# Optimization experiments

Measured on AMD Instinct MI355X. Metric: run time of the kernel, lower is better.

The kernel has to match this reference:

```python
import jax, jax.numpy as jnp
import numpy as np


def conv(x, w, b, stride=1):
    # x: [N,C,H,W], w: [O,I,3,3] (torch OIHW), pad=1
    y = jax.lax.conv_general_dilated(x, w, (stride, stride), ((1, 1), (1, 1)),
                                     dimension_numbers=('NCHW', 'OIHW', 'NCHW'))
    return y + b[None, :, None, None]


def backward_warp(frame, flow):
    # Replicates F.grid_sample(mode='bilinear', padding_mode='border', align_corners=False)
    # with the base grid linspace(-1+1/W, 1-1/W, W) and flow normalized by (W-1)/2, (H-1)/2.
    N, C, H, W = frame.shape
    gx = jnp.linspace(-1.0 + 1.0 / W, 1.0 - 1.0 / W, W, dtype=frame.dtype)[None, None, :] \
         + flow[:, 0] / ((W - 1.0) / 2.0)   # [N,H,W] normalized x
    gy = jnp.linspace(-1.0 + 1.0 / H, 1.0 - 1.0 / H, H, dtype=frame.dtype)[None, :, None] \
         + flow[:, 1] / ((H - 1.0) / 2.0)   # [N,H,W] normalized y
    # align_corners=False un-normalization, then border clamp
    x = jnp.clip(((gx + 1.0) * W - 1.0) / 2.0, 0.0, W - 1.0)
    y = jnp.clip(((gy + 1.0) * H - 1.0) / 2.0, 0.0, H - 1.0)
    x0 = jnp.floor(x); y0 = jnp.floor(y)
    wx = (x - x0)[:, None]; wy = (y - y0)[:, None]   # [N,1,H,W]
    ix0 = x0.astype(jnp.int32); iy0 = y0.astype(jnp.int32)
    ix1 = jnp.minimum(ix0 + 1, W - 1); iy1 = jnp.minimum(iy0 + 1, H - 1)
    gather = jax.vmap(lambda fr, iy, ix: fr[:, iy, ix])  # per-sample [C,H,W] gather
    v00 = gather(frame, iy0, ix0); v01 = gather(frame, iy0, ix1)
    v10 = gather(frame, iy1, ix0); v11 = gather(frame, iy1, ix1)
    return (v00 * (1 - wx) * (1 - wy) + v01 * wx * (1 - wy)
            + v10 * (1 - wx) * wy + v11 * wx * wy)


def up2x(x):
    # F.interpolate(scale_factor=2, mode='bilinear', align_corners=False)
    N, C, H, W = x.shape
    return jax.image.resize(x, (N, C, 2 * H, 2 * W), method='bilinear')


def forward_fn(img0, img1, ft0, ft1, ft0_s2, ft1_s2, ft0_s4, ft1_s4,
               c0_0, c0_1, c0_2, c1_0, c1_1, c1_2,
               wd0a, bd0a, wd0b, bd0b, wd1a, bd1a, wd1b, bd1b,
               wd2a, bd2a, wd2b, bd2b, wu0, bu0, wu1, bu1, wu2, bu2, wfin, bfin):
    relu = jax.nn.relu
    # down0: [N,70,H,W] -> [N,32,H/2,W/2]
    s0_in = jnp.concatenate([img0, img1, backward_warp(c0_0, ft0), backward_warp(c1_0, ft1)], axis=1)
    s0 = relu(conv(relu(conv(s0_in, wd0a, bd0a, 2)), wd0b, bd0b))
    # down1: [N,128,H/2,W/2] -> [N,64,H/4,W/4]
    s1_in = jnp.concatenate([s0, backward_warp(c0_1, ft0_s2), backward_warp(c1_1, ft1_s2)], axis=1)
    s1 = relu(conv(relu(conv(s1_in, wd1a, bd1a, 2)), wd1b, bd1b))
    # down2: [N,192,H/4,W/4] -> [N,96,H/8,W/8]
    s2_in = jnp.concatenate([s1, backward_warp(c0_2, ft0_s4), backward_warp(c1_2, ft1_s4)], axis=1)
    s2 = relu(conv(relu(conv(s2_in, wd2a, bd2a, 2)), wd2b, bd2b))
    # decoder with skip concats; each up block is Sequential(ReLU, Conv, ReLU)
    x = relu(conv(relu(up2x(s2)), wu0, bu0))
    x = relu(conv(relu(up2x(jnp.concatenate([x, s1], axis=1))), wu1, bu1))
    x = relu(conv(relu(up2x(jnp.concatenate([x, s0], axis=1))), wu2, bu2))
    return conv(x, wfin, bfin)  # [N,4,H,W]


def setup_inputs() -> dict:
    key = jax.random.key(0)
    ks = iter(jax.random.split(key, 64))
    N, H, W = 4, 384, 384
    f32 = jnp.float32
    inp = {
        'img0': jax.random.uniform(next(ks), (N, 3, H, W), f32),
        'img1': jax.random.uniform(next(ks), (N, 3, H, W), f32),
        'ft0': jax.random.normal(next(ks), (N, 2, H, W), f32),
        'ft1': jax.random.normal(next(ks), (N, 2, H, W), f32),
        'ft0_s2': jax.random.normal(next(ks), (N, 2, H // 2, W // 2), f32),
        'ft1_s2': jax.random.normal(next(ks), (N, 2, H // 2, W // 2), f32),
        'ft0_s4': jax.random.normal(next(ks), (N, 2, H // 4, W // 4), f32),
        'ft1_s4': jax.random.normal(next(ks), (N, 2, H // 4, W // 4), f32),
        'c0_0': jax.random.normal(next(ks), (N, 32, H, W), f32),
        'c0_1': jax.random.normal(next(ks), (N, 48, H // 2, W // 2), f32),
        'c0_2': jax.random.normal(next(ks), (N, 64, H // 4, W // 4), f32),
        'c1_0': jax.random.normal(next(ks), (N, 32, H, W), f32),
        'c1_1': jax.random.normal(next(ks), (N, 48, H // 2, W // 2), f32),
        'c1_2': jax.random.normal(next(ks), (N, 64, H // 4, W // 4), f32),
    }
    # conv weights, torch OIHW layout; input_dim = 3*2 + 32*2 = 70
    shapes = {
        'wd0a': (32, 70, 3, 3), 'wd0b': (32, 32, 3, 3),
        'wd1a': (64, 128, 3, 3), 'wd1b': (64, 64, 3, 3),
        'wd2a': (96, 192, 3, 3), 'wd2b': (96, 96, 3, 3),
        'wu0': (64, 96, 3, 3), 'wu1': (32, 128, 3, 3), 'wu2': (70, 64, 3, 3),
        'wfin': (4, 70, 3, 3),
    }
    for name, shp in shapes.items():
        fan_in = shp[1] * 9
        inp[name] = jax.random.normal(next(ks), shp, f32) * (1.0 / np.sqrt(fan_in))
        inp['b' + name[1:]] = jax.random.normal(next(ks), (shp[0],), f32) * 0.01
    return inp


def reference(img0, img1, ft0, ft1, ft0_s2, ft1_s2, ft0_s4, ft1_s4,
              c0_0, c0_1, c0_2, c1_0, c1_1, c1_2,
              wd0a, bd0a, wd0b, bd0b, wd1a, bd1a, wd1b, bd1b,
              wd2a, bd2a, wd2b, bd2b, wu0, bu0, wu1, bu1, wu2, bu2, wfin, bfin):
    return forward_fn(img0, img1, ft0, ft1, ft0_s2, ft1_s2, ft0_s4, ft1_s4,
                      c0_0, c0_1, c0_2, c1_0, c1_1, c1_2,
                      wd0a, bd0a, wd0b, bd0b, wd1a, bd1a, wd1b, bd1b,
                      wd2a, bd2a, wd2b, bd2b, wu0, bu0, wu1, bu1, wu2, bu2, wfin, bfin)
```

## Files before the change

kernel.cpp:

```cpp
#include <hip/hip_runtime.h>

#define DIV_UP(a,b) (((a)+(b)-1)/(b))

typedef unsigned short u16;
typedef __attribute__((ext_vector_type(8))) short s8v;
typedef __attribute__((ext_vector_type(4))) float f4v;
typedef __attribute__((ext_vector_type(2))) unsigned int u2v;

__device__ __forceinline__ float b2f(u16 x) {
    return __uint_as_float(((unsigned)x) << 16);
}
__device__ __forceinline__ u16 f2b(float f) {
    unsigned u = __float_as_uint(f);
    return (u16)((u + 0x7FFFu + ((u >> 16) & 1u)) >> 16);
}

#define GLD16(gp, lp) __builtin_amdgcn_global_load_lds( \
    (const __attribute__((address_space(1))) unsigned int*)(gp), \
    (__attribute__((address_space(3))) unsigned int*)(lp), 16, 0, 0)

struct HZ { u16* p; int H, W, C; };
struct HZ6 { HZ d[6]; };
__global__ __launch_bounds__(256) void halo_zero(HZ6 Z)
{
    HZ d = Z.d[blockIdx.y];
    int pw = d.W + 2, ph = d.H + 2;
    int tot = 4 * ph * pw;
    int idx = blockIdx.x * 256 + threadIdx.x;
    if (idx >= tot) return;
    int r = idx % (ph * pw);
    int y = r / pw, x = r - y * pw;
    if (y > 0 && y <= d.H && x > 0 && x <= d.W) return;
    u16* p = d.p + (size_t)idx * d.C;
    s8v z = {0,0,0,0,0,0,0,0};
    for (int c = 0; c < d.C; c += 8) *(s8v*)(p + c) = z;
}

struct WT { const float* src; u16* dst; int Cout, Cin, COUTP, CINP, shift; };
struct WT10 { WT d[10]; };
__global__ __launch_bounds__(256) void wtrans(WT10 Z)
{
    WT d = Z.d[blockIdx.y];
    int tot = 9 * d.COUTP * d.CINP;
    int idx = blockIdx.x * 256 + threadIdx.x;
    if (idx >= tot) return;
    int s = idx / (d.COUTP * d.CINP);
    int r = idx - s * (d.COUTP * d.CINP);
    int co = r / d.CINP, ci = r - co * d.CINP;
    int sci = ci;
    bool ok = (co < d.Cout);
    if (d.shift) {
        if (ci < 6)                 sci = ci;
        else if (ci >= 8 && ci < 72) sci = ci - 2;
        else                        ok = false;
    }
    ok = ok && (sci < d.Cin);
    float v = ok ? d.src[((size_t)co * d.Cin + sci) * 9 + s] : 0.f;
    d.dst[idx] = f2b(v);
}

__global__ __launch_bounds__(256) void img_cat(
    const float* __restrict__ i0, const float* __restrict__ i1, u16* __restrict__ dst)
{
    int idx = blockIdx.x * 256 + threadIdx.x;
    if (idx >= 4 * 147456) return;
    int n = idx / 147456, r = idx - n * 147456;
    int y = r / 384, x = r - y * 384;
    u16* p = dst + ((size_t)n * 386 * 386 + (size_t)(y + 1) * 386 + (x + 1)) * 72;
#pragma unroll
    for (int c = 0; c < 3; ++c) {
        p[c]     = f2b(i0[((size_t)(n * 3 + c)) * 147456 + r]);
        p[3 + c] = f2b(i1[((size_t)(n * 3 + c)) * 147456 + r]);
    }
    p[6] = 0; p[7] = 0;
}

__global__ __launch_bounds__(256) void t_nhwc(
    const float* __restrict__ src, u16* __restrict__ dst, int C, int HW, int total)
{
    int idx = blockIdx.x * 256 + threadIdx.x;
    if (idx >= total) return;
    int n = idx / HW, p = idx - n * HW;
    const float* s = src + (size_t)n * C * HW + p;
    u16* d = dst + (size_t)idx * C;
    for (int c8 = 0; c8 < C; c8 += 8) {
        s8v v;
#pragma unroll
        for (int i = 0; i < 8; ++i)
            v[i] = (short)f2b(s[(size_t)(c8 + i) * HW]);
        *(s8v*)(d + c8) = v;
    }
}

__global__ __launch_bounds__(256) void warp_nhwc(
    const u16* __restrict__ fr, const float* __restrict__ flow,
    u16* __restrict__ dst, int chb, int C, int H, int W, int CALLOC, int total)
{
    int HW = H * W;
    int idx = blockIdx.x * 256 + threadIdx.x;
    if (idx >= total) return;
    int n = idx / HW, r = idx - n * HW;
    int i = r / W, j = r - i * W;

    float fx = flow[((size_t)n * 2 + 0) * HW + r];
    float fy = flow[((size_t)n * 2 + 1) * HW + r];
    float x = (float)j + fx * ((float)W / (float)(W - 1));
    float y = (float)i + fy * ((float)H / (float)(H - 1));
    x = fminf(fmaxf(x, 0.f), (float)(W - 1));
    y = fminf(fmaxf(y, 0.f), (float)(H - 1));
    float x0f = floorf(x), y0f = floorf(y);
    int ix0 = (int)x0f, iy0 = (int)y0f;
    int ix1 = ix0 + 1; if (ix1 > W - 1) ix1 = W - 1;
    int iy1 = iy0 + 1; if (iy1 > H - 1) iy1 = H - 1;
    float wx = x - x0f, wy = y - y0f;
    float w00 = (1.f - wx) * (1.f - wy), w01 = wx * (1.f - wy);
    float w10 = (1.f - wx) * wy,         w11 = wx * wy;

    const u16* fb  = fr + (size_t)n * HW * C;
    const u16* p00 = fb + (size_t)(iy0 * W + ix0) * C;
    const u16* p01 = fb + (size_t)(iy0 * W + ix1) * C;
    const u16* p10 = fb + (size_t)(iy1 * W + ix0) * C;
    const u16* p11 = fb + (size_t)(iy1 * W + ix1) * C;
    u16* db = dst + ((size_t)n * (H + 2) * (W + 2) + (size_t)(i + 1) * (W + 2) + (j + 1)) * CALLOC + chb;

    for (int c8 = 0; c8 < C; c8 += 8) {
        s8v a = *(const s8v*)(p00 + c8);
        s8v b = *(const s8v*)(p01 + c8);
        s8v c = *(const s8v*)(p10 + c8);
        s8v d = *(const s8v*)(p11 + c8);
        s8v o;
#pragma unroll
        for (int t = 0; t < 8; ++t)
            o[t] = (short)f2b(w00 * b2f((u16)a[t]) + w01 * b2f((u16)b[t])
                            + w10 * b2f((u16)c[t]) + w11 * b2f((u16)d[t]));
        *(s8v*)(db + c8) = o;
    }
}

template<int CINP, int CHUNK, int CIN_ALLOC, int COUTP, int COUT, int STORE_LIM,
         int HO, int WO, int HT, int STRIDE, int RELU, int SRC_MODE, int OUT_MODE, int OCALLOC>
__global__ __launch_bounds__(256) void conv_k(
    const u16* __restrict__ srcA, const u16* __restrict__ srcB,
    long nsA, int rsA, int cA, long nsB, int rsB, int cB, int splitC,
    const u16* __restrict__ wt, const float* __restrict__ bias,
    void* __restrict__ outv)
{
    constexpr int WROWS = (HT == 16) ? 4 : 1;
    constexpr int ROWS  = (STRIDE == 1) ? HT + 2 : 2 * HT + 1;
    constexpr int COLS  = (STRIDE == 1) ? 18 : 33;
    constexpr int SUBS  = CHUNK / 8;
    constexpr int LSUB  = (SUBS == 8) ? 3 : 2;
    constexpr int XM    = SUBS - 1;
    constexpr int CH2   = CHUNK * 2;
    constexpr int NCHK  = CINP / CHUNK;
    constexpr int KK    = CHUNK / 32;
    constexpr int MT    = COUTP / 16;
    constexpr int NPX   = ROWS * COLS;
    constexpr int IN_B  = NPX * CH2;
    constexpr int W_B   = COUTP * CH2;
    constexpr int WI    = WO * STRIDE;
    constexpr int Hs    = HO / 2, Ws = WO / 2;
    constexpr long NSO  = (OUT_MODE == 0) ? (long)(HO + 2) * (WO + 2) * OCALLOC
                                          : (long)HO * WO * OCALLOC;

    __shared__ s8v ldsv[(IN_B + 2 * W_B) / 16];
    char* lds  = (char*)ldsv;
    char* ldw0 = lds + IN_B;
    char* ldw1 = ldw0 + W_B;

    const int tid  = threadIdx.x;
    const int wv   = tid >> 6;
    const int lane = tid & 63;
    const int lr   = lane & 15;
    const int koct = lane >> 4;
    const int bx   = blockIdx.x, n = blockIdx.z;
    const int tx   = (bx % (WO / 16)) * 16;
    const int ty   = (bx / (WO / 16)) * HT;

    f4v acc[MT][WROWS];
#pragma unroll
    for (int m = 0; m < MT; ++m)
#pragma unroll
        for (int r = 0; r < WROWS; ++r) acc[m][r] = (f4v){0.f, 0.f, 0.f, 0.f};

    float bv[MT][4];
#pragma unroll
    for (int m = 0; m < MT; ++m)
#pragma unroll
        for (int j = 0; j < 4; ++j) {
            int co = m * 16 + koct * 4 + j;
            bv[m][j] = (co < COUT) ? bias[co] : 0.f;
        }

    for (int cig = 0; cig < NCHK; ++cig) {
        if (cig) __syncthreads();

        if constexpr (SRC_MODE == 0) {
            const u16* ns = srcA + (size_t)n * nsA;
            if (CIN_ALLOC >= CINP || (cig + 1) * CHUNK <= CIN_ALLOC) {
                for (int t = tid; t < NPX * SUBS; t += 256) {
                    int q = t >> LSUB, sub = t & XM;
                    int iy = q / COLS, ix = q - iy * COLS;
                    int xr = (STRIDE == 1) ? (q & XM) : ((q >> 1) & XM);
                    int ci0 = cig * CHUNK + (sub ^ xr) * 8;
                    const u16* g = ns + ((size_t)(ty * STRIDE + iy) * (WI + 2)
                                         + (tx * STRIDE + ix)) * CIN_ALLOC + ci0;
                    GLD16(g, lds + t * 16);
                }
            } else {
                for (int t = tid; t < NPX * SUBS; t += 256) {
                    int q = t >> LSUB, sub = t & XM;
                    int iy = q / COLS, ix = q - iy * COLS;
                    int xr = (STRIDE == 1) ? (q & XM) : ((q >> 1) & XM);
                    int ci0 = cig * CHUNK + (sub ^ xr) * 8;
                    s8v v = {0,0,0,0,0,0,0,0};
                    if (ci0 < CIN_ALLOC)
                        v = *(const s8v*)(ns + ((size_t)(ty * STRIDE + iy) * (WI + 2)
                                                + (tx * STRIDE + ix)) * CIN_ALLOC + ci0);
                    *(s8v*)(lds + t * 16) = v;
                }
            }
        } else {
            for (int t = tid; t < NPX * SUBS; t += 256) {
                int q = t >> LSUB, sub = t & XM;
                int iy = q / COLS, ix = q - iy * COLS;
                int ssub = sub ^ (q & XM);
                int ci0 = cig * CHUNK + ssub * 8;
                int gy = ty + iy - 1, gx = tx + ix - 1;
                s8v val = {0,0,0,0,0,0,0,0};
                if ((unsigned)gy < (unsigned)HO && (unsigned)gx < (unsigned)WO) {
                    const u16* sp; int rs, cal, cof; long nss;
                    if (ci0 < splitC) { sp = srcA; nss = nsA; rs = rsA; cal = cA; cof = ci0; }
                    else              { sp = srcB; nss = nsB; rs = rsB; cal = cB; cof = ci0 - splitC; }
                    sp += (size_t)n * nss;
                    float fy = ((float)gy + 0.5f) * 0.5f - 0.5f;
                    float fx = ((float)gx + 0.5f) * 0.5f - 0.5f;
                    float y0f = floorf(fy), x0f = floorf(fx);
                    float wy = fy - y0f, wx = fx - x0f;
                    int y0 = (int)y0f, x0 = (int)x0f;
                    int y1 = y0 + 1, x1 = x0 + 1;
                    y0 = max(y0, 0); x0 = max(x0, 0);
                    y1 = min(y1, Hs - 1); x1 = min(x1, Ws - 1);
                    const s8v a = *(const s8v*)(sp + (size_t)y0 * rs + (size_t)x0 * cal + cof);
                    const s8v b = *(const s8v*)(sp + (size_t)y0 * rs + (size_t)x1 * cal + cof);
                    const s8v c = *(const s8v*)(sp + (size_t)y1 * rs + (size_t)x0 * cal + cof);
                    const s8v d = *(const s8v*)(sp + (size_t)y1 * rs + (size_t)x1 * cal + cof);
                    float w00 = (1.f - wx) * (1.f - wy), w01 = wx * (1.f - wy);
                    float w10 = (1.f - wx) * wy,         w11 = wx * wy;
#pragma unroll
                    for (int i = 0; i < 8; ++i) {
                        float v = w00 * b2f((u16)a[i]) + w01 * b2f((u16)b[i])
                                + w10 * b2f((u16)c[i]) + w11 * b2f((u16)d[i]);
                        val[i] = (short)f2b(v);
                    }
                }
                *(s8v*)(lds + t * 16) = val;
            }
        }

        auto stageW = [&](int s, char* dstb) {
            for (int t = tid; t < COUTP * SUBS; t += 256) {
                int co = t >> LSUB, sub = t & XM;
                int ssub = sub ^ (co & XM);
                const u16* g = wt + ((size_t)(s * COUTP + co) * CINP + cig * CHUNK + ssub * 8);
                GLD16(g, dstb + t * 16);
            }
        };
        stageW(0, ldw0);

#pragma unroll
        for (int s = 0; s < 9; ++s) {
            __syncthreads();
            if (s < 8) stageW(s + 1, (s & 1) ? ldw0 : ldw1);
            char* wc = (s & 1) ? ldw1 : ldw0;
            const int dy = s / 3, dx = s - dy * 3;
#pragma unroll
            for (int kk = 0; kk < KK; ++kk) {
                const int koff = kk * 64 + koct * 16;
                s8v bfr[WROWS];
#pragma unroll
                for (int r = 0; r < WROWS; ++r) {
                    int orow = wv * WROWS + r;
                    int q, xr;
                    if (STRIDE == 1) { q = (orow + dy) * COLS + lr + dx; xr = q & XM; }
                    else             { q = (2 * orow + dy) * COLS + 2 * lr + dx; xr = (q >> 1) & XM; }
                    bfr[r] = *(const s8v*)(lds + q * CH2 + (koff ^ (xr << 4)));
                }
#pragma unroll
                for (int m = 0; m < MT; ++m) {
                    s8v afr = *(const s8v*)(wc + (m * 16 + lr) * CH2 + (koff ^ ((lr & XM) << 4)));
#pragma unroll
                    for (int r = 0; r < WROWS; ++r)
                        acc[m][r] = __builtin_amdgcn_mfma_f32_16x16x32_bf16(afr, bfr[r], acc[m][r], 0, 0, 0);
                }
            }
        }
    }

#pragma unroll
    for (int m = 0; m < MT; ++m) {
#pragma unroll
        for (int r = 0; r < WROWS; ++r) {
            int row = ty + wv * WROWS + r, col = tx + lr;
            float x0 = acc[m][r][0] + bv[m][0];
            float x1 = acc[m][r][1] + bv[m][1];
            float x2 = acc[m][r][2] + bv[m][2];
            float x3 = acc[m][r][3] + bv[m][3];
            if (RELU) {
                x0 = fmaxf(x0, 0.f); x1 = fmaxf(x1, 0.f);
                x2 = fmaxf(x2, 0.f); x3 = fmaxf(x3, 0.f);
            }
            int co0 = m * 16 + koct * 4;
            if constexpr (OUT_MODE == 2) {
                float* op = (float*)outv;
                float xs[4] = {x0, x1, x2, x3};
#pragma unroll
                for (int j = 0; j < 4; ++j)
                    if (co0 + j < STORE_LIM)
                        op[((size_t)(n * 4 + co0 + j) * HO + row) * WO + col] = xs[j];
            } else {
                size_t pix = (OUT_MODE == 0)
                    ? ((size_t)(row + 1) * (WO + 2) + (col + 1))
                    : ((size_t)row * WO + col);
                u16* ob = (u16*)outv + (size_t)n * NSO + pix * OCALLOC + co0;
                if (co0 + 3 < STORE_LIM) {
                    unsigned lo = (unsigned)f2b(x0) | ((unsigned)f2b(x1) << 16);
                    unsigned hi = (unsigned)f2b(x2) | ((unsigned)f2b(x3) << 16);
                    *(u2v*)ob = (u2v){lo, hi};
                } else {
                    float xs[4] = {x0, x1, x2, x3};
#pragma unroll
                    for (int j = 0; j < 4; ++j)
                        if (co0 + j < STORE_LIM) ob[j] = f2b(xs[j]);
                }
            }
        }
    }
}

extern "C" void kernel_launch(void* const* d_in, const int* in_sizes, int n_in,
                              void* d_out, int out_size, void* d_ws, size_t ws_size,
                              hipStream_t stream)
{
    const float* img0  = (const float*)d_in[0];
    const float* img1  = (const float*)d_in[1];
    const float* ft0   = (const float*)d_in[2];
    const float* ft1   = (const float*)d_in[3];
    const float* ft0s2 = (const float*)d_in[4];
    const float* ft1s2 = (const float*)d_in[5];
    const float* ft0s4 = (const float*)d_in[6];
    const float* ft1s4 = (const float*)d_in[7];
    const float* c0_0  = (const float*)d_in[8];
    const float* c0_1  = (const float*)d_in[9];
    const float* c0_2  = (const float*)d_in[10];
    const float* c1_0  = (const float*)d_in[11];
    const float* c1_1  = (const float*)d_in[12];
    const float* c1_2  = (const float*)d_in[13];
    const float* wd0a = (const float*)d_in[14]; const float* bd0a = (const float*)d_in[15];
    const float* wd0b = (const float*)d_in[16]; const float* bd0b = (const float*)d_in[17];
    const float* wd1a = (const float*)d_in[18]; const float* bd1a = (const float*)d_in[19];
    const float* wd1b = (const float*)d_in[20]; const float* bd1b = (const float*)d_in[21];
    const float* wd2a = (const float*)d_in[22]; const float* bd2a = (const float*)d_in[23];
    const float* wd2b = (const float*)d_in[24]; const float* bd2b = (const float*)d_in[25];
    const float* wu0  = (const float*)d_in[26]; const float* bu0  = (const float*)d_in[27];
    const float* wu1  = (const float*)d_in[28]; const float* bu1  = (const float*)d_in[29];
    const float* wu2  = (const float*)d_in[30]; const float* bu2  = (const float*)d_in[31];
    const float* wfin = (const float*)d_in[32]; const float* bfin = (const float*)d_in[33];

    u16* ws = (u16*)d_ws;
    u16* s0in = ws + 0;
    u16* x2   = ws + 0;
    u16* s1in = ws + 42913152;
    u16* s2in = ws + 62182784;
    u16* scr  = ws + 69558656;
    u16* t0   = ws + 69558656;
    u16* t1   = ws + 74376064;
    u16* t2   = ws + 76834688;
    u16* s2b  = ws + 77794688;
    u16* x0   = ws + 78679424;
    u16* x1   = ws + 81038720;
    u16* wtb  = ws + 85757312;
    u16* Wd0a = wtb;
    u16* Wd0b = Wd0a + 27648;
    u16* Wd1a = Wd0b + 9216;
    u16* Wd1b = Wd1a + 73728;
    u16* Wd2a = Wd1b + 36864;
    u16* Wd2b = Wd2a + 165888;
    u16* Wu0  = Wd2b + 82944;
    u16* Wu1  = Wu0 + 55296;
    u16* Wu2  = Wu1 + 36864;
    u16* Wfin = Wu2 + 46080;

    const int HW384 = 147456, HW192 = 36864, HW96 = 9216;

    for (int f = 0; f < 2; ++f) {
        const float* fr = f ? c1_0 : c0_0;
        const float* fl = f ? ft1 : ft0;
        int chb = f ? 40 : 8;
        for (int n = 0; n < 4; ++n) {
            t_nhwc<<<DIV_UP(HW384, 256), 256, 0, stream>>>(
                fr + (size_t)n * 32 * HW384, scr, 32, HW384, HW384);
            warp_nhwc<<<DIV_UP(HW384, 256), 256, 0, stream>>>(
                scr, fl + (size_t)n * 2 * HW384,
                s0in + (size_t)n * 386 * 386 * 72, chb, 32, 384, 384, 72, HW384);
        }
    }
    for (int f = 0; f < 2; ++f) {
        t_nhwc<<<DIV_UP(4 * HW192, 256), 256, 0, stream>>>(
            f ? c1_1 : c0_1, scr, 48, HW192, 4 * HW192);
        warp_nhwc<<<DIV_UP(4 * HW192, 256), 256, 0, stream>>>(
            scr, f ? ft1s2 : ft0s2, s1in, f ? 80 : 32, 48, 192, 192, 128, 4 * HW192);
    }
    for (int f = 0; f < 2; ++f) {
        t_nhwc<<<DIV_UP(4 * HW96, 256), 256, 0, stream>>>(
            f ? c1_2 : c0_2, scr, 64, HW96, 4 * HW96);
        warp_nhwc<<<DIV_UP(4 * HW96, 256), 256, 0, stream>>>(
            scr, f ? ft1s4 : ft0s4, s2in, f ? 128 : 64, 64, 96, 96, 192, 4 * HW96);
    }

    HZ6 hz = {{ {s0in, 384, 384, 72}, {s1in, 192, 192, 128}, {s2in, 96, 96, 192},
                {t0, 192, 192, 32},   {t1, 96, 96, 64},      {t2, 48, 48, 96} }};
    halo_zero<<<dim3(DIV_UP(4 * 386 * 386, 256), 6), 256, 0, stream>>>(hz);

    WT10 wt = {{ {wd0a, Wd0a, 32, 70, 32, 96, 1},  {wd0b, Wd0b, 32, 32, 32, 32, 0},
                 {wd1a, Wd1a, 64, 128, 64, 128, 0},{wd1b, Wd1b, 64, 64, 64, 64, 0},
                 {wd2a, Wd2a, 96, 192, 96, 192, 0},{wd2b, Wd2b, 96, 96, 96, 96, 0},
                 {wu0,  Wu0,  64, 96, 64, 96, 0},  {wu1,  Wu1,  32, 128, 32, 128, 0},
                 {wu2,  Wu2,  70, 64, 80, 64, 0},  {wfin, Wfin, 4, 70, 16, 96, 0} }};
    wtrans<<<dim3(DIV_UP(9 * 96 * 192, 256), 10), 256, 0, stream>>>(wt);

    img_cat<<<DIV_UP(4 * 147456, 256), 256, 0, stream>>>(img0, img1, s0in);

    conv_k<96,32,72, 32,32,32, 192,192,4,2,1, 0,0,32>
        <<<dim3(12*48,1,4),256,0,stream>>>(s0in,nullptr, 386L*386*72,0,0, 0,0,0,0, Wd0a,bd0a,t0);
    conv_k<32,32,32, 32,32,32, 192,192,16,1,1, 0,0,128>
        <<<dim3(12*12,1,4),256,0,stream>>>(t0,nullptr, 194L*194*32,0,0, 0,0,0,0, Wd0b,bd0b,s1in);

    conv_k<128,32,128, 64,64,64, 96,96,4,2,1, 0,0,64>
        <<<dim3(6*24,1,4),256,0,stream>>>(s1in,nullptr, 194L*194*128,0,0, 0,0,0,0, Wd1a,bd1a,t1);
    conv_k<64,64,64, 64,64,64, 96,96,4,1,1, 0,0,192>
        <<<dim3(6*24,1,4),256,0,stream>>>(t1,nullptr, 98L*98*64,0,0, 0,0,0,0, Wd1b,bd1b,s2in);

    conv_k<192,32,192, 96,96,96, 48,48,4,2,1, 0,0,96>
        <<<dim3(3*12,1,4),256,0,stream>>>(s2in,nullptr, 98L*98*192,0,0, 0,0,0,0, Wd2a,bd2a,t2);
    conv_k<96,32,96, 96,96,96, 48,48,4,1,1, 0,1,96>
        <<<dim3(3*12,1,4),256,0,stream>>>(t2,nullptr, 50L*50*96,0,0, 0,0,0,0, Wd2b,bd2b,s2b);

    conv_k<96,32,96, 64,64,64, 96,96,4,1,1, 1,1,64>
        <<<dim3(6*24,1,4),256,0,stream>>>(s2b,s2b, 48L*48*96,48*96,96, 48L*48*96,48*96,96, 96,
                                          Wu0,bu0,x0);
    conv_k<128,64,128, 32,32,32, 192,192,16,1,1, 1,1,32>
        <<<dim3(12*12,1,4),256,0,stream>>>(x0, s2in + (size_t)(98+1)*192,
                                           96L*96*64,96*64,64, 98L*98*192,98*192,192, 64,
                                           Wu1,bu1,x1);
    conv_k<64,64,64, 80,70,70, 384,384,16,1,1, 1,0,72>
        <<<dim3(24*24,1,4),256,0,stream>>>(x1, s1in + (size_t)(194+1)*128,
                                           192L*192*32,192*32,32, 194L*194*128,194*128,128, 32,
                                           Wu2,bu2,x2);

    conv_k<96,32,72, 16,4,4, 384,384,16,1,0, 0,2,0>
        <<<dim3(24*24,1,4),256,0,stream>>>(x2,nullptr, 386L*386*72,0,0, 0,0,0,0, Wfin,bfin,d_out);
}
```

Measured before the change: 797.7 us.

## Materialize upsampled inputs and read conv weights directly from global memory

Moves the bilinear 2x upsample and skip-concatenation out of the conv loader into a separate kernel that writes a zero-padded upsampled buffer, so the up-path convs use the plain padded loader. It also removes the double-buffered LDS staging of weights: MFMA A-fragments are now loaded straight from global memory, with one barrier per channel chunk instead of one per tap. The intent is to cut loader arithmetic and synchronisation. In exchange it adds large intermediate write/read traffic and uncached global weight reads inside the inner loop.

```diff
diff --git a/kernel.cpp b/kernel.cpp
--- a/kernel.cpp
+++ b/kernel.cpp
@@ -137,11 +137,56 @@
     }
 }
 
+__global__ __launch_bounds__(256) void up2x_mat(
+    const u16* __restrict__ A, long nsA, int rsA, int cA,
+    const u16* __restrict__ B, long nsB, int rsB, int cB, int splitC,
+    u16* __restrict__ out, int C, int Hs, int Ws)
+{
+    int Ho = 2 * Hs, Wo = 2 * Ws;
+    int pw = Wo + 2, ph = Ho + 2;
+    int tot = 4 * ph * pw;
+    int idx = blockIdx.x * 256 + threadIdx.x;
+    if (idx >= tot) return;
+    int n = idx / (ph * pw), r = idx - n * (ph * pw);
+    int py = r / pw, px = r - py * pw;
+    u16* d = out + (size_t)idx * C;
+    int gy = py - 1, gx = px - 1;
+    if ((unsigned)gy >= (unsigned)Ho || (unsigned)gx >= (unsigned)Wo) {
+        s8v z = {0,0,0,0,0,0,0,0};
+        for (int c8 = 0; c8 < C; c8 += 8) *(s8v*)(d + c8) = z;
+        return;
+    }
+    float fy = ((float)gy + 0.5f) * 0.5f - 0.5f;
+    float fx = ((float)gx + 0.5f) * 0.5f - 0.5f;
+    float y0f = floorf(fy), x0f = floorf(fx);
+    float wy = fy - y0f, wx = fx - x0f;
+    int y0 = max((int)y0f, 0), x0 = max((int)x0f, 0);
+    int y1 = min((int)y0f + 1, Hs - 1), x1 = min((int)x0f + 1, Ws - 1);
+    float w00 = (1.f - wx) * (1.f - wy), w01 = wx * (1.f - wy);
+    float w10 = (1.f - wx) * wy,         w11 = wx * wy;
+
+    for (int c8 = 0; c8 < C; c8 += 8) {
+        const u16* sp; int rs, cal, cof; long nss;
+        if (c8 < splitC) { sp = A; nss = nsA; rs = rsA; cal = cA; cof = c8; }
+        else              { sp = B; nss = nsB; rs = rsB; cal = cB; cof = c8 - splitC; }
+        sp += (size_t)n * nss;
+        const s8v a = *(const s8v*)(sp + (size_t)y0 * rs + (size_t)x0 * cal + cof);
+        const s8v b = *(const s8v*)(sp + (size_t)y0 * rs + (size_t)x1 * cal + cof);
+        const s8v c = *(const s8v*)(sp + (size_t)y1 * rs + (size_t)x0 * cal + cof);
+        const s8v e = *(const s8v*)(sp + (size_t)y1 * rs + (size_t)x1 * cal + cof);
+        s8v o;
+#pragma unroll
+        for (int i = 0; i < 8; ++i)
+            o[i] = (short)f2b(w00 * b2f((u16)a[i]) + w01 * b2f((u16)b[i])
+                            + w10 * b2f((u16)c[i]) + w11 * b2f((u16)e[i]));
+        *(s8v*)(d + c8) = o;
+    }
+}
+
 template<int CINP, int CHUNK, int CIN_ALLOC, int COUTP, int COUT, int STORE_LIM,
          int HO, int WO, int HT, int STRIDE, int RELU, int SRC_MODE, int OUT_MODE, int OCALLOC>
 __global__ __launch_bounds__(256) void conv_k(
-    const u16* __restrict__ srcA, const u16* __restrict__ srcB,
-    long nsA, int rsA, int cA, long nsB, int rsB, int cB, int splitC,
+    const u16* __restrict__ src, long ns,
     const u16* __restrict__ wt, const float* __restrict__ bias,
     void* __restrict__ outv)
 {
@@ -157,16 +202,12 @@
     constexpr int MT    = COUTP / 16;
     constexpr int NPX   = ROWS * COLS;
     constexpr int IN_B  = NPX * CH2;
-    constexpr int W_B   = COUTP * CH2;
     constexpr int WI    = WO * STRIDE;
-    constexpr int Hs    = HO / 2, Ws = WO / 2;
     constexpr long NSO  = (OUT_MODE == 0) ? (long)(HO + 2) * (WO + 2) * OCALLOC
                                           : (long)HO * WO * OCALLOC;
 
-    __shared__ s8v ldsv[(IN_B + 2 * W_B) / 16];
-    char* lds  = (char*)ldsv;
-    char* ldw0 = lds + IN_B;
-    char* ldw1 = ldw0 + W_B;
+    __shared__ s8v ldsv[IN_B / 16];
+    char* lds = (char*)ldsv;
 
     const int tid  = threadIdx.x;
     const int wv   = tid >> 6;
@@ -195,16 +236,16 @@
     for (int cig = 0; cig < NCHK; ++cig) {
         if (cig) __syncthreads();
 
+        const u16* nsrc = src + (size_t)n * ns;
         if constexpr (SRC_MODE == 0) {
-            const u16* ns = srcA + (size_t)n * nsA;
             if (CIN_ALLOC >= CINP || (cig + 1) * CHUNK <= CIN_ALLOC) {
                 for (int t = tid; t < NPX * SUBS; t += 256) {
                     int q = t >> LSUB, sub = t & XM;
                     int iy = q / COLS, ix = q - iy * COLS;
                     int xr = (STRIDE == 1) ? (q & XM) : ((q >> 1) & XM);
                     int ci0 = cig * CHUNK + (sub ^ xr) * 8;
-                    const u16* g = ns + ((size_t)(ty * STRIDE + iy) * (WI + 2)
-                                         + (tx * STRIDE + ix)) * CIN_ALLOC + ci0;
+                    const u16* g = nsrc + ((size_t)(ty * STRIDE + iy) * (WI + 2)
+                                           + (tx * STRIDE + ix)) * CIN_ALLOC + ci0;
                     GLD16(g, lds + t * 16);
                 }
             } else {
@@ -215,8 +256,8 @@
                     int ci0 = cig * CHUNK + (sub ^ xr) * 8;
                     s8v v = {0,0,0,0,0,0,0,0};
                     if (ci0 < CIN_ALLOC)
-                        v = *(const s8v*)(ns + ((size_t)(ty * STRIDE + iy) * (WI + 2)
-                                                + (tx * STRIDE + ix)) * CIN_ALLOC + ci0);
+                        v = *(const s8v*)(nsrc + ((size_t)(ty * STRIDE + iy) * (WI + 2)
+                                                  + (tx * STRIDE + ix)) * CIN_ALLOC + ci0);
                     *(s8v*)(lds + t * 16) = v;
                 }
             }
@@ -224,56 +265,20 @@
             for (int t = tid; t < NPX * SUBS; t += 256) {
                 int q = t >> LSUB, sub = t & XM;
                 int iy = q / COLS, ix = q - iy * COLS;
-                int ssub = sub ^ (q & XM);
-                int ci0 = cig * CHUNK + ssub * 8;
+                int xr = q & XM;
+                int ci0 = cig * CHUNK + (sub ^ xr) * 8;
                 int gy = ty + iy - 1, gx = tx + ix - 1;
-                s8v val = {0,0,0,0,0,0,0,0};
-                if ((unsigned)gy < (unsigned)HO && (unsigned)gx < (unsigned)WO) {
-                    const u16* sp; int rs, cal, cof; long nss;
-                    if (ci0 < splitC) { sp = srcA; nss = nsA; rs = rsA; cal = cA; cof = ci0; }
-                    else              { sp = srcB; nss = nsB; rs = rsB; cal = cB; cof = ci0 - splitC; }
-                    sp += (size_t)n * nss;
-                    float fy = ((float)gy + 0.5f) * 0.5f - 0.5f;
-                    float fx = ((float)gx + 0.5f) * 0.5f - 0.5f;
-                    float y0f = floorf(fy), x0f = floorf(fx);
-                    float wy = fy - y0f, wx = fx - x0f;
-                    int y0 = (int)y0f, x0 = (int)x0f;
-                    int y1 = y0 + 1, x1 = x0 + 1;
-                    y0 = max(y0, 0); x0 = max(x0, 0);
-                    y1 = min(y1, Hs - 1); x1 = min(x1, Ws - 1);
-                    const s8v a = *(const s8v*)(sp + (size_t)y0 * rs + (size_t)x0 * cal + cof);
-                    const s8v b = *(const s8v*)(sp + (size_t)y0 * rs + (size_t)x1 * cal + cof);
-                    const s8v c = *(const s8v*)(sp + (size_t)y1 * rs + (size_t)x0 * cal + cof);
-                    const s8v d = *(const s8v*)(sp + (size_t)y1 * rs + (size_t)x1 * cal + cof);
-                    float w00 = (1.f - wx) * (1.f - wy), w01 = wx * (1.f - wy);
-                    float w10 = (1.f - wx) * wy,         w11 = wx * wy;
-#pragma unroll
-                    for (int i = 0; i < 8; ++i) {
-                        float v = w00 * b2f((u16)a[i]) + w01 * b2f((u16)b[i])
-                                + w10 * b2f((u16)c[i]) + w11 * b2f((u16)d[i]);
-                        val[i] = (short)f2b(v);
-                    }
-                }
-                *(s8v*)(lds + t * 16) = val;
+                s8v v = {0,0,0,0,0,0,0,0};
+                if ((unsigned)gy < (unsigned)HO && (unsigned)gx < (unsigned)WO && ci0 < CIN_ALLOC)
+                    v = *(const s8v*)(nsrc + ((size_t)gy * WO + gx) * CIN_ALLOC + ci0);
+                *(s8v*)(lds + t * 16) = v;
             }
         }
-
-        auto stageW = [&](int s, char* dstb) {
-            for (int t = tid; t < COUTP * SUBS; t += 256) {
-                int co = t >> LSUB, sub = t & XM;
-                int ssub = sub ^ (co & XM);
-                const u16* g = wt + ((size_t)(s * COUTP + co) * CINP + cig * CHUNK + ssub * 8);
-                GLD16(g, dstb + t * 16);
-            }
-        };
-        stageW(0, ldw0);
-
-#pragma unroll
+        __syncthreads();
+
         for (int s = 0; s < 9; ++s) {
-            __syncthreads();
-            if (s < 8) stageW(s + 1, (s & 1) ? ldw0 : ldw1);
-            char* wc = (s & 1) ? ldw1 : ldw0;
             const int dy = s / 3, dx = s - dy * 3;
+            const u16* wbase = wt + (size_t)(s * COUTP) * CINP + cig * CHUNK;
 #pragma unroll
             for (int kk = 0; kk < KK; ++kk) {
                 const int koff = kk * 64 + koct * 16;
@@ -288,7 +293,8 @@
                 }
 #pragma unroll
                 for (int m = 0; m < MT; ++m) {
-                    s8v afr = *(const s8v*)(wc + (m * 16 + lr) * CH2 + (koff ^ ((lr & XM) << 4)));
+                    s8v afr = *(const s8v*)(wbase + (size_t)(m * 16 + lr) * CINP
+                                            + kk * 32 + koct * 8);
 #pragma unroll
                     for (int r = 0; r < WROWS; ++r)
                         acc[m][r] = __builtin_amdgcn_mfma_f32_16x16x32_bf16(afr, bfr[r], acc[m][r], 0, 0, 0);
@@ -369,7 +375,8 @@
 
     u16* ws = (u16*)d_ws;
     u16* s0in = ws + 0;
-    u16* x2   = ws + 0;
+    u16* upb  = ws + 0;
+    u16* x2   = ws + 42913152;
     u16* s1in = ws + 42913152;
     u16* s2in = ws + 62182784;
     u16* scr  = ws + 69558656;
@@ -432,32 +439,37 @@
     img_cat<<<DIV_UP(4 * 147456, 256), 256, 0, stream>>>(img0, img1, s0in);
 
     conv_k<96,32,72, 32,32,32, 192,192,4,2,1, 0,0,32>
-        <<<dim3(12*48,1,4),256,0,stream>>>(s0in,nullptr, 386L*386*72,0,0, 0,0,0,0, Wd0a,bd0a,t0);
+        <<<dim3(12*48,1,4),256,0,stream>>>(s0in, 386L*386*72, Wd0a, bd0a, t0);
     conv_k<32,32,32, 32,32,32, 192,192,16,1,1, 0,0,128>
-        <<<dim3(12*12,1,4),256,0,stream>>>(t0,nullptr, 194L*194*32,0,0, 0,0,0,0, Wd0b,bd0b,s1in);
+        <<<dim3(12*12,1,4),256,0,stream>>>(t0, 194L*194*32, Wd0b, bd0b, s1in);
 
     conv_k<128,32,128, 64,64,64, 96,96,4,2,1, 0,0,64>
-        <<<dim3(6*24,1,4),256,0,stream>>>(s1in,nullptr, 194L*194*128,0,0, 0,0,0,0, Wd1a,bd1a,t1);
+        <<<dim3(6*24,1,4),256,0,stream>>>(s1in, 194L*194*128, Wd1a, bd1a, t1);
     conv_k<64,64,64, 64,64,64, 96,96,4,1,1, 0,0,192>
-        <<<dim3(6*24,1,4),256,0,stream>>>(t1,nullptr, 98L*98*64,0,0, 0,0,0,0, Wd1b,bd1b,s2in);
+        <<<dim3(6*24,1,4),256,0,stream>>>(t1, 98L*98*64, Wd1b, bd1b, s2in);
 
     conv_k<192,32,192, 96,96,96, 48,48,4,2,1, 0,0,96>
-        <<<dim3(3*12,1,4),256,0,stream>>>(s2in,nullptr, 98L*98*192,0,0, 0,0,0,0, Wd2a,bd2a,t2);
+        <<<dim3(3*12,1,4),256,0,stream>>>(s2in, 98L*98*192, Wd2a, bd2a, t2);
     conv_k<96,32,96, 96,96,96, 48,48,4,1,1, 0,1,96>
-        <<<dim3(3*12,1,4),256,0,stream>>>(t2,nullptr, 50L*50*96,0,0, 0,0,0,0, Wd2b,bd2b,s2b);
-
-    conv_k<96,32,96, 64,64,64, 96,96,4,1,1, 1,1,64>
-        <<<dim3(6*24,1,4),256,0,stream>>>(s2b,s2b, 48L*48*96,48*96,96, 48L*48*96,48*96,96, 96,
-                                          Wu0,bu0,x0);
-    conv_k<128,64,128, 32,32,32, 192,192,16,1,1, 1,1,32>
-        <<<dim3(12*12,1,4),256,0,stream>>>(x0, s2in + (size_t)(98+1)*192,
-                                           96L*96*64,96*64,64, 98L*98*192,98*192,192, 64,
-                                           Wu1,bu1,x1);
-    conv_k<64,64,64, 80,70,70, 384,384,16,1,1, 1,0,72>
-        <<<dim3(24*24,1,4),256,0,stream>>>(x1, s1in + (size_t)(194+1)*128,
-                                           192L*192*32,192*32,32, 194L*194*128,194*128,128, 32,
-                                           Wu2,bu2,x2);
-
-    conv_k<96,32,72, 16,4,4, 384,384,16,1,0, 0,2,0>
-        <<<dim3(24*24,1,4),256,0,stream>>>(x2,nullptr, 386L*386*72,0,0, 0,0,0,0, Wfin,bfin,d_out);
-}
+        <<<dim3(3*12,1,4),256,0,stream>>>(t2, 50L*50*96, Wd2b, bd2b, s2b);
+
+    up2x_mat<<<DIV_UP(4*98*98, 256), 256, 0, stream>>>(
+        s2b, 48L*48*96, 48*96, 96, nullptr, 0, 0, 0, 96, upb, 96, 48, 48);
+    conv_k<96,32,96, 64,64,64, 96,96,4,1,1, 0,1,64>
+        <<<dim3(6*24,1,4),256,0,stream>>>(upb, 98L*98*96, Wu0, bu0, x0);
+
+    up2x_mat<<<DIV_UP(4*194*194, 256), 256, 0, stream>>>(
+        x0, 96L*96*64, 96*64, 64, s2in + (size_t)(98+1)*192, 98L*98*192, 98*192, 192, 64,
+        upb, 128, 96, 96);
+    conv_k<128,64,128, 32,32,32, 192,192,16,1,1, 0,1,32>
+        <<<dim3(12*12,1,4),256,0,stream>>>(upb, 194L*194*128, Wu1, bu1, x1);
+
+    up2x_mat<<<DIV_UP(4*386*386, 256), 256, 0, stream>>>(
+        x1, 192L*192*32, 192*32, 32, s1in + (size_t)(194+1)*128, 194L*194*128, 194*128, 128, 32,
+        upb, 64, 192, 192);
+    conv_k<64,64,64, 80,70,70, 384,384,16,1,1, 0,1,72>
+        <<<dim3(24*24,1,4),256,0,stream>>>(upb, 386L*386*64, Wu2, bu2, x2);
+
+    conv_k<96,32,72, 16,4,4, 384,384,16,1,0, 2,2,0>
+        <<<dim3(24*24,1,4),256,0,stream>>>(x2, 384L*384*72, Wfin, bfin, d_out);
+}
```

Result: slower. 1.113 ms (+39.5%).

## Materialize upsampled skip-concat buffer before up2 conv, read final conv unpadded

Applied to the files above, without the earlier changes.

Adds a standalone up2x_mat kernel that writes the bilinear 2x upsample of x1, concatenated with the s1in skip channels, into a zero-padded bf16 buffer. The up2 conv then stages its input with async global-to-LDS loads (SRC_MODE 0) instead of interpolating inside every tile's staging loop. The up2 conv now writes an unpadded output, and the final conv gets a new SRC_MODE 2 that handles borders with bounds checks. This removes redundant per-tile interpolation work and synchronous loads, at the cost of an extra full-resolution write and read of a 64-channel intermediate and one more kernel launch.

```diff
diff --git a/kernel.cpp b/kernel.cpp
--- a/kernel.cpp
+++ b/kernel.cpp
@@ -134,6 +134,52 @@
             o[t] = (short)f2b(w00 * b2f((u16)a[t]) + w01 * b2f((u16)b[t])
                             + w10 * b2f((u16)c[t]) + w11 * b2f((u16)d[t]));
         *(s8v*)(db + c8) = o;
+    }
+}
+
+__global__ __launch_bounds__(256) void up2x_mat(
+    const u16* __restrict__ A, long nsA, int rsA, int cA,
+    const u16* __restrict__ B, long nsB, int rsB, int cB, int splitC,
+    u16* __restrict__ out, int C, int Hs, int Ws)
+{
+    int Ho = 2 * Hs, Wo = 2 * Ws;
+    int pw = Wo + 2, ph = Ho + 2;
+    int tot = 4 * ph * pw;
+    int idx = blockIdx.x * 256 + threadIdx.x;
+    if (idx >= tot) return;
+    int n = idx / (ph * pw), r = idx - n * (ph * pw);
+    int py = r / pw, px = r - py * pw;
+    u16* d = out + (size_t)idx * C;
+    int gy = py - 1, gx = px - 1;
+    if ((unsigned)gy >= (unsigned)Ho || (unsigned)gx >= (unsigned)Wo) {
+        s8v z = {0,0,0,0,0,0,0,0};
+        for (int c8 = 0; c8 < C; c8 += 8) *(s8v*)(d + c8) = z;
+        return;
+    }
+    float fy = ((float)gy + 0.5f) * 0.5f - 0.5f;
+    float fx = ((float)gx + 0.5f) * 0.5f - 0.5f;
+    float y0f = floorf(fy), x0f = floorf(fx);
+    float wy = fy - y0f, wx = fx - x0f;
+    int y0 = max((int)y0f, 0), x0 = max((int)x0f, 0);
+    int y1 = min((int)y0f + 1, Hs - 1), x1 = min((int)x0f + 1, Ws - 1);
+    float w00 = (1.f - wx) * (1.f - wy), w01 = wx * (1.f - wy);
+    float w10 = (1.f - wx) * wy,         w11 = wx * wy;
+
+    for (int c8 = 0; c8 < C; c8 += 8) {
+        const u16* sp; int rs, cal, cof; long nss;
+        if (c8 < splitC) { sp = A; nss = nsA; rs = rsA; cal = cA; cof = c8; }
+        else              { sp = B; nss = nsB; rs = rsB; cal = cB; cof = c8 - splitC; }
+        sp += (size_t)n * nss;
+        const s8v a = *(const s8v*)(sp + (size_t)y0 * rs + (size_t)x0 * cal + cof);
+        const s8v b = *(const s8v*)(sp + (size_t)y0 * rs + (size_t)x1 * cal + cof);
+        const s8v c = *(const s8v*)(sp + (size_t)y1 * rs + (size_t)x0 * cal + cof);
+        const s8v e = *(const s8v*)(sp + (size_t)y1 * rs + (size_t)x1 * cal + cof);
+        s8v o;
+#pragma unroll
+        for (int i = 0; i < 8; ++i)
+            o[i] = (short)f2b(w00 * b2f((u16)a[i]) + w01 * b2f((u16)b[i])
+                            + w10 * b2f((u16)c[i]) + w11 * b2f((u16)e[i]));
+        *(s8v*)(d + c8) = o;
     }
 }
 
@@ -220,7 +266,7 @@
                     *(s8v*)(lds + t * 16) = v;
                 }
             }
-        } else {
+        } else if constexpr (SRC_MODE == 1) {
             for (int t = tid; t < NPX * SUBS; t += 256) {
                 int q = t >> LSUB, sub = t & XM;
                 int iy = q / COLS, ix = q - iy * COLS;
@@ -256,6 +302,32 @@
                 }
                 *(s8v*)(lds + t * 16) = val;
             }
+        } else {
+            const u16* ns = srcA + (size_t)n * nsA;
+            const bool interior = (ty >= 1) && (ty + ROWS - 2 <= HO - 1)
+                               && (tx >= 1) && (tx + COLS - 2 <= WO - 1);
+            if (interior && (CIN_ALLOC >= CINP || (cig + 1) * CHUNK <= CIN_ALLOC)) {
+                for (int t = tid; t < NPX * SUBS; t += 256) {
+                    int q = t >> LSUB, sub = t & XM;
+                    int iy = q / COLS, ix = q - iy * COLS;
+                    int xr = q & XM;
+                    int ci0 = cig * CHUNK + (sub ^ xr) * 8;
+                    const u16* g = ns + ((size_t)(ty + iy - 1) * WO + (tx + ix - 1)) * CIN_ALLOC + ci0;
+                    GLD16(g, lds + t * 16);
+                }
+            } else {
+                for (int t = tid; t < NPX * SUBS; t += 256) {
+                    int q = t >> LSUB, sub = t & XM;
+                    int iy = q / COLS, ix = q - iy * COLS;
+                    int xr = q & XM;
+                    int ci0 = cig * CHUNK + (sub ^ xr) * 8;
+                    int gy = ty + iy - 1, gx = tx + ix - 1;
+                    s8v v = {0,0,0,0,0,0,0,0};
+                    if ((unsigned)gy < (unsigned)HO && (unsigned)gx < (unsigned)WO && ci0 < CIN_ALLOC)
+                        v = *(const s8v*)(ns + ((size_t)gy * WO + gx) * CIN_ALLOC + ci0);
+                    *(s8v*)(lds + t * 16) = v;
+                }
+            }
         }
 
         auto stageW = [&](int s, char* dstb) {
@@ -369,8 +441,9 @@
 
     u16* ws = (u16*)d_ws;
     u16* s0in = ws + 0;
-    u16* x2   = ws + 0;
+    u16* upb3 = ws + 0;
     u16* s1in = ws + 42913152;
+    u16* x2   = ws + 42913152;
     u16* s2in = ws + 62182784;
     u16* scr  = ws + 69558656;
     u16* t0   = ws + 69558656;
@@ -453,11 +526,13 @@
         <<<dim3(12*12,1,4),256,0,stream>>>(x0, s2in + (size_t)(98+1)*192,
                                            96L*96*64,96*64,64, 98L*98*192,98*192,192, 64,
                                            Wu1,bu1,x1);
-    conv_k<64,64,64, 80,70,70, 384,384,16,1,1, 1,0,72>
-        <<<dim3(24*24,1,4),256,0,stream>>>(x1, s1in + (size_t)(194+1)*128,
-                                           192L*192*32,192*32,32, 194L*194*128,194*128,128, 32,
-                                           Wu2,bu2,x2);
-
-    conv_k<96,32,72, 16,4,4, 384,384,16,1,0, 0,2,0>
-        <<<dim3(24*24,1,4),256,0,stream>>>(x2,nullptr, 386L*386*72,0,0, 0,0,0,0, Wfin,bfin,d_out);
-}
+
+    up2x_mat<<<DIV_UP(4*386*386, 256), 256, 0, stream>>>(
+        x1, 192L*192*32, 192*32, 32, s1in + (size_t)(194+1)*128, 194L*194*128, 194*128, 128, 32,
+        upb3, 64, 192, 192);
+    conv_k<64,64,64, 80,70,70, 384,384,16,1,1, 0,1,72>
+        <<<dim3(24*24,1,4),256,0,stream>>>(upb3,nullptr, 386L*386*64,0,0, 0,0,0,0, Wu2,bu2,x2);
+
+    conv_k<96,32,72, 16,4,4, 384,384,16,1,0, 2,2,0>
+        <<<dim3(24*24,1,4),256,0,stream>>>(x2,nullptr, 384L*384*72,0,0, 0,0,0,0, Wfin,bfin,d_out);
+}
```

Measured after the change: 859.1 us. 1.08x slower.

## Batch level-0 warp launches, specialize 2x upsample weights, shrink wu2 tile height

Applied to the files above, without the earlier changes.

Merges the per-sample transpose and warp launches at full resolution into one batched launch per frame. It uses a larger scratch buffer aliased onto the s1in region, which is free at that point. The fused 2x bilinear upsample in the conv loader now computes indices and weights with integer bit operations and constant 0.25/0.75 weights instead of float floor math. The wu2 conv drops from 16-row to 8-row tiles (WROWS generalized to HT/4), doubling the grid to improve occupancy and load balance at the cost of more halo reloads and weight restaging.

```diff
diff --git a/kernel.cpp b/kernel.cpp
--- a/kernel.cpp
+++ b/kernel.cpp
@@ -145,7 +145,7 @@
     const u16* __restrict__ wt, const float* __restrict__ bias,
     void* __restrict__ outv)
 {
-    constexpr int WROWS = (HT == 16) ? 4 : 1;
+    constexpr int WROWS = HT / 4;
     constexpr int ROWS  = (STRIDE == 1) ? HT + 2 : 2 * HT + 1;
     constexpr int COLS  = (STRIDE == 1) ? 18 : 33;
     constexpr int SUBS  = CHUNK / 8;
@@ -233,14 +233,12 @@
                     if (ci0 < splitC) { sp = srcA; nss = nsA; rs = rsA; cal = cA; cof = ci0; }
                     else              { sp = srcB; nss = nsB; rs = rsB; cal = cB; cof = ci0 - splitC; }
                     sp += (size_t)n * nss;
-                    float fy = ((float)gy + 0.5f) * 0.5f - 0.5f;
-                    float fx = ((float)gx + 0.5f) * 0.5f - 0.5f;
-                    float y0f = floorf(fy), x0f = floorf(fx);
-                    float wy = fy - y0f, wx = fx - x0f;
-                    int y0 = (int)y0f, x0 = (int)x0f;
-                    int y1 = y0 + 1, x1 = x0 + 1;
-                    y0 = max(y0, 0); x0 = max(x0, 0);
-                    y1 = min(y1, Hs - 1); x1 = min(x1, Ws - 1);
+                    int y0 = (gy >> 1) + (gy & 1) - 1;
+                    int x0 = (gx >> 1) + (gx & 1) - 1;
+                    float wy = (gy & 1) ? 0.25f : 0.75f;
+                    float wx = (gx & 1) ? 0.25f : 0.75f;
+                    int y1 = min(y0 + 1, Hs - 1); y0 = max(y0, 0);
+                    int x1 = min(x0 + 1, Ws - 1); x0 = max(x0, 0);
                     const s8v a = *(const s8v*)(sp + (size_t)y0 * rs + (size_t)x0 * cal + cof);
                     const s8v b = *(const s8v*)(sp + (size_t)y0 * rs + (size_t)x1 * cal + cof);
                     const s8v c = *(const s8v*)(sp + (size_t)y1 * rs + (size_t)x0 * cal + cof);
@@ -371,6 +369,7 @@
     u16* s0in = ws + 0;
     u16* x2   = ws + 0;
     u16* s1in = ws + 42913152;
+    u16* scrB = ws + 42913152;
     u16* s2in = ws + 62182784;
     u16* scr  = ws + 69558656;
     u16* t0   = ws + 69558656;
@@ -394,16 +393,10 @@
     const int HW384 = 147456, HW192 = 36864, HW96 = 9216;
 
     for (int f = 0; f < 2; ++f) {
-        const float* fr = f ? c1_0 : c0_0;
-        const float* fl = f ? ft1 : ft0;
-        int chb = f ? 40 : 8;
-        for (int n = 0; n < 4; ++n) {
-            t_nhwc<<<DIV_UP(HW384, 256), 256, 0, stream>>>(
-                fr + (size_t)n * 32 * HW384, scr, 32, HW384, HW384);
-            warp_nhwc<<<DIV_UP(HW384, 256), 256, 0, stream>>>(
-                scr, fl + (size_t)n * 2 * HW384,
-                s0in + (size_t)n * 386 * 386 * 72, chb, 32, 384, 384, 72, HW384);
-        }
+        t_nhwc<<<DIV_UP(4 * HW384, 256), 256, 0, stream>>>(
+            f ? c1_0 : c0_0, scrB, 32, HW384, 4 * HW384);
+        warp_nhwc<<<DIV_UP(4 * HW384, 256), 256, 0, stream>>>(
+            scrB, f ? ft1 : ft0, s0in, f ? 40 : 8, 32, 384, 384, 72, 4 * HW384);
     }
     for (int f = 0; f < 2; ++f) {
         t_nhwc<<<DIV_UP(4 * HW192, 256), 256, 0, stream>>>(
@@ -453,8 +446,8 @@
         <<<dim3(12*12,1,4),256,0,stream>>>(x0, s2in + (size_t)(98+1)*192,
                                            96L*96*64,96*64,64, 98L*98*192,98*192,192, 64,
                                            Wu1,bu1,x1);
-    conv_k<64,64,64, 80,70,70, 384,384,16,1,1, 1,0,72>
-        <<<dim3(24*24,1,4),256,0,stream>>>(x1, s1in + (size_t)(194+1)*128,
+    conv_k<64,64,64, 80,70,70, 384,384,8,1,1, 1,0,72>
+        <<<dim3(24*48,1,4),256,0,stream>>>(x1, s1in + (size_t)(194+1)*128,
                                            192L*192*32,192*32,32, 194L*194*128,194*128,128, 32,
                                            Wu2,bu2,x2);
 
```

Result: faster. 745.9 us (-6.5%).
